# Optimization experiments

Hardware: AMD Instinct MI355X
Metric: run time of the kernel (lower is better)

The kernel has to match this reference:

```python
import jax, jax.numpy as jnp
import numpy as np

B, C, H, W = 2, 256, 32, 32
PK, CK = 256, 256


def setup_inputs() -> dict:
    key = jax.random.key(0)
    ks = jax.random.split(key, 9)
    s = 1.0 / np.sqrt(C)
    return {
        'x': jax.random.normal(ks[0], (B, C, H, W), jnp.float32),
        'primary_indices': jax.random.randint(ks[1], (B, PK), 0, B * H * W),
        'compare_indices': jax.random.randint(ks[2], (B, CK), 0, B * H * W),
        'pre_w': jax.random.uniform(ks[3], (3, C, C), jnp.float32, -s, s),
        'pre_b': jax.random.uniform(ks[4], (3, C), jnp.float32, -s, s),
        'post_w': jax.random.uniform(ks[5], (2, C, C), jnp.float32, -s, s),
        'post_b': jax.random.uniform(ks[6], (2, C), jnp.float32, -s, s),
        'post_out_w': jax.random.uniform(ks[7], (2, C), jnp.float32, -s, s),
        'post_out_b': jax.random.uniform(ks[8], (2,), jnp.float32, -s, s),
    }


def reference(x, primary_indices, compare_indices, pre_w, pre_b,
              post_w, post_b, post_out_w, post_out_b):
    # pre_compare: stack of 1x1 convs (c->c->c->c), ReLU between layers
    h = x
    for i in range(3):
        h = jnp.einsum('bchw,oc->bohw', h, pre_w[i]) + pre_b[i][None, :, None, None]
        if i < 2:
            h = jax.nn.relu(h)
    bs, c, hh, ww = h.shape
    # flatten to [bs*h*w, c] node features (matches torch transpose+reshape)
    flat = h.reshape(bs, c, hh * ww).transpose(0, 2, 1).reshape(bs * hh * ww, c)
    # gather primary / compare node features with global flat indices
    xp = flat[primary_indices.reshape(-1)].reshape(bs, -1, c).transpose(0, 2, 1)  # [b,c,pk]
    xc = flat[compare_indices.reshape(-1)].reshape(bs, -1, c).transpose(0, 2, 1)  # [b,c,ck]
    # broadcast pairwise squared difference -> [b,c,pk,ck]
    xx = (xp[:, :, :, None] - xc[:, :, None, :]) ** 2
    # post_compare: 1x1 conv stack c->c->c->2, ReLU between layers
    g = xx
    for i in range(2):
        g = jax.nn.relu(jnp.einsum('bcpq,oc->bopq', g, post_w[i]) + post_b[i][None, :, None, None])
    out = jnp.einsum('bcpq,oc->bopq', g, post_out_w) + post_out_b[None, :, None, None]
    return out  # [b, 2, pk, ck]
```

## Files before the change

kernel.cpp:

```cpp
#include <hip/hip_runtime.h>

typedef unsigned short u16;
typedef short bf16x8 __attribute__((ext_vector_type(8)));
typedef float f32x4 __attribute__((ext_vector_type(4)));
typedef u16 u16x4 __attribute__((ext_vector_type(4)));

__device__ __forceinline__ float b2f(u16 h) {
  unsigned u = ((unsigned)h) << 16;
  return __builtin_bit_cast(float, u);
}
__device__ __forceinline__ u16 f2b(float f) {
  return __builtin_bit_cast(u16, (__bf16)f);
}
__device__ __forceinline__ void gld_lds16(const void* g, void* l) {
  __builtin_amdgcn_global_load_lds(
      (__attribute__((address_space(1))) void*)(g),
      (__attribute__((address_space(3))) void*)(l), 16, 0, 0);
}

__global__ void dense_edge_prep(const float* __restrict__ x,
                                const float* __restrict__ pre_w,
                                const float* __restrict__ post_w,
                                u16* __restrict__ wb, u16* __restrict__ xt) {
  const int blk = blockIdx.x;
  const int t = threadIdx.x;
  if (blk < 160) {
    const int id = blk * 256 + t;
    const int layer = id >> 13;
    const int sid = id & 8191;
    const int m = sid >> 5;
    const int s8 = sid & 31;
    const float* src = (layer < 2) ? (post_w + layer * 65536)
                                   : (pre_w + (layer - 2) * 65536);
    u16* dst = wb + layer * 65536;
    f32x4 a = *(const f32x4*)(src + m * 256 + s8 * 8);
    f32x4 c = *(const f32x4*)(src + m * 256 + s8 * 8 + 4);
    bf16x8 o;
#pragma unroll
    for (int j = 0; j < 4; j++) o[j] = (short)f2b(a[j]);
#pragma unroll
    for (int j = 0; j < 4; j++) o[4 + j] = (short)f2b(c[j]);
    *(bf16x8*)(dst + (s8 * 256 + m) * 8) = o;
  } else {
    __shared__ float tile[32 * 65];
    const int xb = blk - 160;
    const int b = xb >> 7;
    const int ct = (xb >> 4) & 7;
    const int ht = xb & 15;
    const int c0 = ct * 32, hw0 = ht * 64;
#pragma unroll
    for (int rep = 0; rep < 8; rep++) {
      const int idx = rep * 256 + t;
      const int cl = idx >> 6, hl = idx & 63;
      tile[cl * 65 + hl] = x[(b * 256 + c0 + cl) * 1024 + hw0 + hl];
    }
    __syncthreads();
    const int hl = t >> 2, c8 = t & 3;
    bf16x8 o;
#pragma unroll
    for (int i = 0; i < 8; i++) o[i] = (short)f2b(tile[(c8 * 8 + i) * 65 + hl]);
    *(bf16x8*)(xt + (b * 1024 + hw0 + hl) * 256 + c0 + c8 * 8) = o;
  }
}

__global__ __launch_bounds__(256, 2) void dense_edge_pre(
    const u16* __restrict__ xt, const u16* __restrict__ wpre,
    const float* __restrict__ preb, u16* __restrict__ flat) {
  __shared__ u16 feat[2][4096];
  const int t = threadIdx.x;
  const int wv = t >> 6, ln = t & 63;
  const int nb = blockIdx.x * 16;
  const int q4 = ln >> 4, r15 = ln & 15;

#pragma unroll
  for (int i = 0; i < 2; i++) {
    const int slot = wv * 128 + i * 64 + ln;
    const int s8 = slot >> 4, nl = slot & 15;
    gld_lds16(xt + (nb + nl) * 256 + s8 * 8, &feat[0][slot * 8]);
  }
  __syncthreads();

#pragma unroll
  for (int l = 0; l < 3; l++) {
    const u16* wl = wpre + l * 65536;
    f32x4 acc[4];
    f32x4 zero = {0.f, 0.f, 0.f, 0.f};
#pragma unroll
    for (int mt = 0; mt < 4; mt++) acc[mt] = zero;
#pragma unroll
    for (int s = 0; s < 8; s++) {
      bf16x8 bv = *(const bf16x8*)(&feat[l & 1][((s * 4 + q4) * 16 + r15) * 8]);
#pragma unroll
      for (int mt = 0; mt < 4; mt++) {
        bf16x8 av = *(const bf16x8*)(wl + ((s * 4 + q4) * 256 + wv * 64 + mt * 16 + r15) * 8);
        acc[mt] = __builtin_amdgcn_mfma_f32_16x16x32_bf16(av, bv, acc[mt], 0, 0, 0);
      }
    }
    if (l < 2) {
#pragma unroll
      for (int mt = 0; mt < 4; mt++) {
        const int o = wv * 64 + mt * 16 + q4 * 4;
        f32x4 bb = *(const f32x4*)(preb + l * 256 + o);
        u16x4 pk;
#pragma unroll
        for (int r = 0; r < 4; r++) {
          float v = fmaxf(acc[mt][r] + bb[r], 0.f);
          pk[r] = f2b(v);
        }
        *(u16x4*)(&feat[(l + 1) & 1][((o >> 3) * 16 + r15) * 8 + (o & 7)]) = pk;
      }
      __syncthreads();
    } else {
#pragma unroll
      for (int mt = 0; mt < 4; mt++) {
        const int o = wv * 64 + mt * 16 + q4 * 4;
        f32x4 bb = *(const f32x4*)(preb + 512 + o);
        u16x4 pk;
#pragma unroll
        for (int r = 0; r < 4; r++) pk[r] = f2b(acc[mt][r] + bb[r]);
        *(u16x4*)(flat + (nb + r15) * 256 + o) = pk;
      }
    }
  }
}

#define NT 8
__global__ __launch_bounds__(512, 2) void dense_edge_main(
    const u16* __restrict__ flat, const int* __restrict__ pidx,
    const int* __restrict__ cidx, const u16* __restrict__ w1s,
    const u16* __restrict__ w2s, const float* __restrict__ b1,
    const float* __restrict__ b2, const float* __restrict__ w3,
    const float* __restrict__ b3, float* __restrict__ out) {
  __shared__ u16 xxbuf[2][16384];
  __shared__ u16 t1buf[2][16384];
  __shared__ u16 pstage[2048];
  __shared__ u16 qstage[2][2048];
  __shared__ float pbuf[2][8][2][64];

  const int t = threadIdx.x;
  const int wv = t >> 6;
  const int ln = t & 63;
  const int q4 = ln >> 4, r15 = ln & 15;
  const int blk = blockIdx.x;
  const int tile0 = blk * NT;
  const int b = tile0 >> 10;
  const int pt = (tile0 >> 5) & 31;
  const int qt0 = tile0 & 31;
  const int p0 = pt * 8;

  bf16x8 w1f[2][8], w2f[2][8];
#pragma unroll
  for (int s = 0; s < 8; s++)
#pragma unroll
    for (int mt = 0; mt < 2; mt++) {
      const int off = ((s * 4 + q4) * 256 + wv * 32 + mt * 16 + r15) * 8;
      w1f[mt][s] = *(const bf16x8*)(w1s + off);
      w2f[mt][s] = *(const bf16x8*)(w2s + off);
    }

  {
    const int slot = (wv & 3) * 64 + ln;
    const int row = slot & 7, cc = slot >> 3;
    if (wv < 4) {
      const int pn = pidx[b * 256 + p0 + row];
      gld_lds16(flat + pn * 256 + cc * 8, &pstage[slot * 8]);
    } else {
      const int qn = cidx[b * 256 + qt0 * 8 + row];
      gld_lds16(flat + qn * 256 + cc * 8, &qstage[0][slot * 8]);
    }
  }
  __syncthreads();

  const int prow = ln >> 3, qrow = ln & 7;

  {
    const u16* qs = qstage[0];
#pragma unroll
    for (int i = 0; i < 4; i++) {
      const int cc = wv * 4 + i;
      bf16x8 av = *(const bf16x8*)(&pstage[(cc * 8 + prow) * 8]);
      bf16x8 bv = *(const bf16x8*)(&qs[(cc * 8 + qrow) * 8]);
      bf16x8 ov;
#pragma unroll
      for (int jj = 0; jj < 8; jj++) {
        float d = b2f((u16)av[jj]) - b2f((u16)bv[jj]);
        ov[jj] = (short)f2b(d * d);
      }
      *(bf16x8*)(&xxbuf[0][(cc * 64 + ln) * 8]) = ov;
    }
    if (wv >= 4) {
      const int slot = (wv - 4) * 64 + ln;
      const int qn = cidx[b * 256 + (qt0 + 1) * 8 + (slot & 7)];
      gld_lds16(flat + qn * 256 + (slot >> 3) * 8, &qstage[1][slot * 8]);
    }
  }
  __syncthreads();

#pragma unroll 1
  for (int j = 0; j <= NT; j++) {
    if (j < NT - 1) {
      const u16* qs = qstage[(j + 1) & 1];
#pragma unroll
      for (int i = 0; i < 4; i++) {
        const int cc = wv * 4 + i;
        bf16x8 av = *(const bf16x8*)(&pstage[(cc * 8 + prow) * 8]);
        bf16x8 bv = *(const bf16x8*)(&qs[(cc * 8 + qrow) * 8]);
        bf16x8 ov;
#pragma unroll
        for (int jj = 0; jj < 8; jj++) {
          float d = b2f((u16)av[jj]) - b2f((u16)bv[jj]);
          ov[jj] = (short)f2b(d * d);
        }
        *(bf16x8*)(&xxbuf[(j + 1) & 1][(cc * 64 + ln) * 8]) = ov;
      }
    }
    if (j < NT - 2 && wv >= 4) {
      const int slot = (wv - 4) * 64 + ln;
      const int qn = cidx[b * 256 + (qt0 + j + 2) * 8 + (slot & 7)];
      gld_lds16(flat + qn * 256 + (slot >> 3) * 8,
                &qstage[(j + 2) & 1][slot * 8]);
    }
    if (j < NT) {
      const u16* xb = xxbuf[j & 1];
      f32x4 acc[2][4];
      {
        f32x4 zero = {0.f, 0.f, 0.f, 0.f};
#pragma unroll
        for (int mt = 0; mt < 2; mt++)
#pragma unroll
          for (int nt = 0; nt < 4; nt++) acc[mt][nt] = zero;
      }
#pragma unroll
      for (int s = 0; s < 8; s++) {
        bf16x8 bfr[4];
#pragma unroll
        for (int nt = 0; nt < 4; nt++)
          bfr[nt] = *(const bf16x8*)(xb + ((s * 4 + q4) * 64 + nt * 16 + r15) * 8);
#pragma unroll
        for (int mt = 0; mt < 2; mt++)
#pragma unroll
          for (int nt = 0; nt < 4; nt++)
            acc[mt][nt] = __builtin_amdgcn_mfma_f32_16x16x32_bf16(w1f[mt][s], bfr[nt], acc[mt][nt], 0, 0, 0);
      }
#pragma unroll
      for (int mt = 0; mt < 2; mt++) {
        const int o = wv * 32 + mt * 16 + q4 * 4;
        f32x4 bb = *(const f32x4*)(b1 + o);
#pragma unroll
        for (int nt = 0; nt < 4; nt++) {
          const int nn = nt * 16 + r15;
          u16x4 pk;
#pragma unroll
          for (int r = 0; r < 4; r++) {
            float v = fmaxf(acc[mt][nt][r] + bb[r], 0.f);
            pk[r] = f2b(v);
          }
          *(u16x4*)(&t1buf[j & 1][((o >> 3) * 64 + nn) * 8 + (o & 7)]) = pk;
        }
      }
    }
    if (j > 0) {
      const int jm = j - 1;
      const u16* tb = t1buf[jm & 1];
      f32x4 acc[2][4];
      {
        f32x4 zero = {0.f, 0.f, 0.f, 0.f};
#pragma unroll
        for (int mt = 0; mt < 2; mt++)
#pragma unroll
          for (int nt = 0; nt < 4; nt++) acc[mt][nt] = zero;
      }
#pragma unroll
      for (int s = 0; s < 8; s++) {
        bf16x8 bfr[4];
#pragma unroll
        for (int nt = 0; nt < 4; nt++)
          bfr[nt] = *(const bf16x8*)(tb + ((s * 4 + q4) * 64 + nt * 16 + r15) * 8);
#pragma unroll
        for (int mt = 0; mt < 2; mt++)
#pragma unroll
          for (int nt = 0; nt < 4; nt++)
            acc[mt][nt] = __builtin_amdgcn_mfma_f32_16x16x32_bf16(w2f[mt][s], bfr[nt], acc[mt][nt], 0, 0, 0);
      }
      float part[2][4] = {{0.f, 0.f, 0.f, 0.f}, {0.f, 0.f, 0.f, 0.f}};
#pragma unroll
      for (int mt = 0; mt < 2; mt++) {
        const int o = wv * 32 + mt * 16 + q4 * 4;
        f32x4 bb = *(const f32x4*)(b2 + o);
        f32x4 w3a = *(const f32x4*)(w3 + o);
        f32x4 w3b = *(const f32x4*)(w3 + 256 + o);
#pragma unroll
        for (int nt = 0; nt < 4; nt++) {
#pragma unroll
          for (int r = 0; r < 4; r++) {
            float v = fmaxf(acc[mt][nt][r] + bb[r], 0.f);
            part[0][nt] += v * w3a[r];
            part[1][nt] += v * w3b[r];
          }
        }
      }
#pragma unroll
      for (int o3 = 0; o3 < 2; o3++)
#pragma unroll
        for (int nt = 0; nt < 4; nt++) {
          part[o3][nt] += __shfl_xor(part[o3][nt], 16, 64);
          part[o3][nt] += __shfl_xor(part[o3][nt], 32, 64);
        }
      if (q4 == 0) {
#pragma unroll
        for (int o3 = 0; o3 < 2; o3++)
#pragma unroll
          for (int nt = 0; nt < 4; nt++)
            pbuf[jm & 1][wv][o3][nt * 16 + r15] = part[o3][nt];
      }
    }
    if (j >= 2 && t < 128) {
      const int jo = j - 2;
      const int o3 = t >> 6;
      const int n = t & 63;
      float v = b3[o3];
#pragma unroll
      for (int k = 0; k < 8; k++) v += pbuf[jo & 1][k][o3][n];
      out[((b * 2 + o3) * 256 + p0 + (n >> 3)) * 256 + (qt0 + jo) * 8 + (n & 7)] = v;
    }
    __syncthreads();
  }

  if (t < 128) {
    const int jo = NT - 1;
    const int o3 = t >> 6;
    const int n = t & 63;
    float v = b3[o3];
#pragma unroll
    for (int k = 0; k < 8; k++) v += pbuf[jo & 1][k][o3][n];
    out[((b * 2 + o3) * 256 + p0 + (n >> 3)) * 256 + (qt0 + jo) * 8 + (n & 7)] = v;
  }
}

extern "C" void kernel_launch(void* const* d_in, const int* in_sizes, int n_in,
                              void* d_out, int out_size, void* d_ws, size_t ws_size,
                              hipStream_t stream) {
  (void)in_sizes; (void)n_in; (void)out_size; (void)ws_size;
  const float* x          = (const float*)d_in[0];
  const int*   pidx       = (const int*)d_in[1];
  const int*   cidx       = (const int*)d_in[2];
  const float* pre_w      = (const float*)d_in[3];
  const float* pre_b      = (const float*)d_in[4];
  const float* post_w     = (const float*)d_in[5];
  const float* post_b     = (const float*)d_in[6];
  const float* post_out_w = (const float*)d_in[7];
  const float* post_out_b = (const float*)d_in[8];
  float* out = (float*)d_out;

  u16* ws   = (u16*)d_ws;
  u16* wb   = ws;
  u16* w1s  = wb;
  u16* w2s  = wb + 65536;
  u16* wpre = wb + 131072;
  u16* xt   = ws + 327680;
  u16* flat = ws + 851968;

  dense_edge_prep<<<416, 256, 0, stream>>>(x, pre_w, post_w, wb, xt);
  dense_edge_pre<<<128, 256, 0, stream>>>(xt, wpre, pre_b, flat);
  dense_edge_main<<<256, 512, 0, stream>>>(flat, pidx, cidx, w1s, w2s,
                                           post_b, post_b + 256,
                                           post_out_w, post_out_b, out);
}
```

Baseline: 119.5 us.

## Stagger per-wave stage order, raise MFMA priority, and prefetch gather indices

The loop body is split into squared-difference, first GEMM and second GEMM stages. Odd and even waves now run these stages in opposite order, so MFMA-heavy and VALU/LDS-heavy work from different waves can overlap. MFMA loops are wrapped in s_setprio, the primary-row LDS reads are hoisted into registers once, and compare indices are preloaded into registers one step ahead, so the async gather no longer waits on an index load. This costs extra registers and makes per-wave timing between barriers less uniform.

```diff
diff --git a/kernel.cpp b/kernel.cpp
--- a/kernel.cpp
+++ b/kernel.cpp
@@ -158,27 +158,36 @@
       w2f[mt][s] = *(const bf16x8*)(w2s + off);
     }
 
-  {
-    const int slot = (wv & 3) * 64 + ln;
-    const int row = slot & 7, cc = slot >> 3;
-    if (wv < 4) {
-      const int pn = pidx[b * 256 + p0 + row];
-      gld_lds16(flat + pn * 256 + cc * 8, &pstage[slot * 8]);
-    } else {
-      const int qn = cidx[b * 256 + qt0 * 8 + row];
-      gld_lds16(flat + qn * 256 + cc * 8, &qstage[0][slot * 8]);
-    }
+  const int slot4 = (wv & 3) * 64 + ln;
+  const int srow = slot4 & 7, scc = slot4 >> 3;
+  if (wv < 4) {
+    const int pn = pidx[b * 256 + p0 + srow];
+    gld_lds16(flat + pn * 256 + scc * 8, &pstage[slot4 * 8]);
+  } else {
+    const int qn = cidx[b * 256 + qt0 * 8 + srow];
+    gld_lds16(flat + qn * 256 + scc * 8, &qstage[0][slot4 * 8]);
+  }
+  int qn_pro = 0, qn_cur = 0;
+  if (wv >= 4) {
+    qn_pro = cidx[b * 256 + (qt0 + 1) * 8 + srow];
+    qn_cur = cidx[b * 256 + (qt0 + 2) * 8 + srow];
   }
   __syncthreads();
 
   const int prow = ln >> 3, qrow = ln & 7;
 
-  {
-    const u16* qs = qstage[0];
+  bf16x8 pa[4];
+#pragma unroll
+  for (int i = 0; i < 4; i++)
+    pa[i] = *(const bf16x8*)(&pstage[((wv * 4 + i) * 8 + prow) * 8]);
+
+  auto do_xx = [&](int jx) {
+    const u16* qs = qstage[jx & 1];
+    u16* xb = xxbuf[jx & 1];
 #pragma unroll
     for (int i = 0; i < 4; i++) {
       const int cc = wv * 4 + i;
-      bf16x8 av = *(const bf16x8*)(&pstage[(cc * 8 + prow) * 8]);
+      bf16x8 av = pa[i];
       bf16x8 bv = *(const bf16x8*)(&qs[(cc * 8 + qrow) * 8]);
       bf16x8 ov;
 #pragma unroll
@@ -186,134 +195,115 @@
         float d = b2f((u16)av[jj]) - b2f((u16)bv[jj]);
         ov[jj] = (short)f2b(d * d);
       }
-      *(bf16x8*)(&xxbuf[0][(cc * 64 + ln) * 8]) = ov;
-    }
-    if (wv >= 4) {
-      const int slot = (wv - 4) * 64 + ln;
-      const int qn = cidx[b * 256 + (qt0 + 1) * 8 + (slot & 7)];
-      gld_lds16(flat + qn * 256 + (slot >> 3) * 8, &qstage[1][slot * 8]);
-    }
-  }
+      *(bf16x8*)(&xb[(cc * 64 + ln) * 8]) = ov;
+    }
+  };
+
+  auto do_g1 = [&](int jg) {
+    const u16* xb = xxbuf[jg & 1];
+    f32x4 acc[2][4];
+    {
+      f32x4 zero = {0.f, 0.f, 0.f, 0.f};
+#pragma unroll
+      for (int mt = 0; mt < 2; mt++)
+#pragma unroll
+        for (int nt = 0; nt < 4; nt++) acc[mt][nt] = zero;
+    }
+    __builtin_amdgcn_s_setprio(1);
+#pragma unroll
+    for (int s = 0; s < 8; s++) {
+      bf16x8 bfr[4];
+#pragma unroll
+      for (int nt = 0; nt < 4; nt++)
+        bfr[nt] = *(const bf16x8*)(xb + ((s * 4 + q4) * 64 + nt * 16 + r15) * 8);
+#pragma unroll
+      for (int mt = 0; mt < 2; mt++)
+#pragma unroll
+        for (int nt = 0; nt < 4; nt++)
+          acc[mt][nt] = __builtin_amdgcn_mfma_f32_16x16x32_bf16(w1f[mt][s], bfr[nt], acc[mt][nt], 0, 0, 0);
+    }
+    __builtin_amdgcn_s_setprio(0);
+#pragma unroll
+    for (int mt = 0; mt < 2; mt++) {
+      const int o = wv * 32 + mt * 16 + q4 * 4;
+      f32x4 bb = *(const f32x4*)(b1 + o);
+#pragma unroll
+      for (int nt = 0; nt < 4; nt++) {
+        const int nn = nt * 16 + r15;
+        u16x4 pk;
+#pragma unroll
+        for (int r = 0; r < 4; r++) {
+          float v = fmaxf(acc[mt][nt][r] + bb[r], 0.f);
+          pk[r] = f2b(v);
+        }
+        *(u16x4*)(&t1buf[jg & 1][((o >> 3) * 64 + nn) * 8 + (o & 7)]) = pk;
+      }
+    }
+  };
+
+  auto do_g2 = [&](int jg) {
+    const u16* tb = t1buf[jg & 1];
+    f32x4 acc[2][4];
+    {
+      f32x4 zero = {0.f, 0.f, 0.f, 0.f};
+#pragma unroll
+      for (int mt = 0; mt < 2; mt++)
+#pragma unroll
+        for (int nt = 0; nt < 4; nt++) acc[mt][nt] = zero;
+    }
+    __builtin_amdgcn_s_setprio(1);
+#pragma unroll
+    for (int s = 0; s < 8; s++) {
+      bf16x8 bfr[4];
+#pragma unroll
+      for (int nt = 0; nt < 4; nt++)
+        bfr[nt] = *(const bf16x8*)(tb + ((s * 4 + q4) * 64 + nt * 16 + r15) * 8);
+#pragma unroll
+      for (int mt = 0; mt < 2; mt++)
+#pragma unroll
+        for (int nt = 0; nt < 4; nt++)
+          acc[mt][nt] = __builtin_amdgcn_mfma_f32_16x16x32_bf16(w2f[mt][s], bfr[nt], acc[mt][nt], 0, 0, 0);
+    }
+    __builtin_amdgcn_s_setprio(0);
+    float part[2][4] = {{0.f, 0.f, 0.f, 0.f}, {0.f, 0.f, 0.f, 0.f}};
+#pragma unroll
+    for (int mt = 0; mt < 2; mt++) {
+      const int o = wv * 32 + mt * 16 + q4 * 4;
+      f32x4 bb = *(const f32x4*)(b2 + o);
+      f32x4 w3a = *(const f32x4*)(w3 + o);
+      f32x4 w3b = *(const f32x4*)(w3 + 256 + o);
+#pragma unroll
+      for (int nt = 0; nt < 4; nt++) {
+#pragma unroll
+        for (int r = 0; r < 4; r++) {
+          float v = fmaxf(acc[mt][nt][r] + bb[r], 0.f);
+          part[0][nt] += v * w3a[r];
+          part[1][nt] += v * w3b[r];
+        }
+      }
+    }
+#pragma unroll
+    for (int o3 = 0; o3 < 2; o3++)
+#pragma unroll
+      for (int nt = 0; nt < 4; nt++) {
+        part[o3][nt] += __shfl_xor(part[o3][nt], 16, 64);
+        part[o3][nt] += __shfl_xor(part[o3][nt], 32, 64);
+      }
+    if (q4 == 0) {
+#pragma unroll
+      for (int o3 = 0; o3 < 2; o3++)
+#pragma unroll
+        for (int nt = 0; nt < 4; nt++)
+          pbuf[jg & 1][wv][o3][nt * 16 + r15] = part[o3][nt];
+    }
+  };
+
+  do_xx(0);
+  if (wv >= 4) gld_lds16(flat + qn_pro * 256 + scc * 8, &qstage[1][slot4 * 8]);
   __syncthreads();
 
 #pragma unroll 1
   for (int j = 0; j <= NT; j++) {
-    if (j < NT - 1) {
-      const u16* qs = qstage[(j + 1) & 1];
-#pragma unroll
-      for (int i = 0; i < 4; i++) {
-        const int cc = wv * 4 + i;
-        bf16x8 av = *(const bf16x8*)(&pstage[(cc * 8 + prow) * 8]);
-        bf16x8 bv = *(const bf16x8*)(&qs[(cc * 8 + qrow) * 8]);
-        bf16x8 ov;
-#pragma unroll
-        for (int jj = 0; jj < 8; jj++) {
-          float d = b2f((u16)av[jj]) - b2f((u16)bv[jj]);
-          ov[jj] = (short)f2b(d * d);
-        }
-        *(bf16x8*)(&xxbuf[(j + 1) & 1][(cc * 64 + ln) * 8]) = ov;
-      }
-    }
-    if (j < NT - 2 && wv >= 4) {
-      const int slot = (wv - 4) * 64 + ln;
-      const int qn = cidx[b * 256 + (qt0 + j + 2) * 8 + (slot & 7)];
-      gld_lds16(flat + qn * 256 + (slot >> 3) * 8,
-                &qstage[(j + 2) & 1][slot * 8]);
-    }
-    if (j < NT) {
-      const u16* xb = xxbuf[j & 1];
-      f32x4 acc[2][4];
-      {
-        f32x4 zero = {0.f, 0.f, 0.f, 0.f};
-#pragma unroll
-        for (int mt = 0; mt < 2; mt++)
-#pragma unroll
-          for (int nt = 0; nt < 4; nt++) acc[mt][nt] = zero;
-      }
-#pragma unroll
-      for (int s = 0; s < 8; s++) {
-        bf16x8 bfr[4];
-#pragma unroll
-        for (int nt = 0; nt < 4; nt++)
-          bfr[nt] = *(const bf16x8*)(xb + ((s * 4 + q4) * 64 + nt * 16 + r15) * 8);
-#pragma unroll
-        for (int mt = 0; mt < 2; mt++)
-#pragma unroll
-          for (int nt = 0; nt < 4; nt++)
-            acc[mt][nt] = __builtin_amdgcn_mfma_f32_16x16x32_bf16(w1f[mt][s], bfr[nt], acc[mt][nt], 0, 0, 0);
-      }
-#pragma unroll
-      for (int mt = 0; mt < 2; mt++) {
-        const int o = wv * 32 + mt * 16 + q4 * 4;
-        f32x4 bb = *(const f32x4*)(b1 + o);
-#pragma unroll
-        for (int nt = 0; nt < 4; nt++) {
-          const int nn = nt * 16 + r15;
-          u16x4 pk;
-#pragma unroll
-          for (int r = 0; r < 4; r++) {
-            float v = fmaxf(acc[mt][nt][r] + bb[r], 0.f);
-            pk[r] = f2b(v);
-          }
-          *(u16x4*)(&t1buf[j & 1][((o >> 3) * 64 + nn) * 8 + (o & 7)]) = pk;
-        }
-      }
-    }
-    if (j > 0) {
-      const int jm = j - 1;
-      const u16* tb = t1buf[jm & 1];
-      f32x4 acc[2][4];
-      {
-        f32x4 zero = {0.f, 0.f, 0.f, 0.f};
-#pragma unroll
-        for (int mt = 0; mt < 2; mt++)
-#pragma unroll
-          for (int nt = 0; nt < 4; nt++) acc[mt][nt] = zero;
-      }
-#pragma unroll
-      for (int s = 0; s < 8; s++) {
-        bf16x8 bfr[4];
-#pragma unroll
-        for (int nt = 0; nt < 4; nt++)
-          bfr[nt] = *(const bf16x8*)(tb + ((s * 4 + q4) * 64 + nt * 16 + r15) * 8);
-#pragma unroll
-        for (int mt = 0; mt < 2; mt++)
-#pragma unroll
-          for (int nt = 0; nt < 4; nt++)
-            acc[mt][nt] = __builtin_amdgcn_mfma_f32_16x16x32_bf16(w2f[mt][s], bfr[nt], acc[mt][nt], 0, 0, 0);
-      }
-      float part[2][4] = {{0.f, 0.f, 0.f, 0.f}, {0.f, 0.f, 0.f, 0.f}};
-#pragma unroll
-      for (int mt = 0; mt < 2; mt++) {
-        const int o = wv * 32 + mt * 16 + q4 * 4;
-        f32x4 bb = *(const f32x4*)(b2 + o);
-        f32x4 w3a = *(const f32x4*)(w3 + o);
-        f32x4 w3b = *(const f32x4*)(w3 + 256 + o);
-#pragma unroll
-        for (int nt = 0; nt < 4; nt++) {
-#pragma unroll
-          for (int r = 0; r < 4; r++) {
-            float v = fmaxf(acc[mt][nt][r] + bb[r], 0.f);
-            part[0][nt] += v * w3a[r];
-            part[1][nt] += v * w3b[r];
-          }
-        }
-      }
-#pragma unroll
-      for (int o3 = 0; o3 < 2; o3++)
-#pragma unroll
-        for (int nt = 0; nt < 4; nt++) {
-          part[o3][nt] += __shfl_xor(part[o3][nt], 16, 64);
-          part[o3][nt] += __shfl_xor(part[o3][nt], 32, 64);
-        }
-      if (q4 == 0) {
-#pragma unroll
-        for (int o3 = 0; o3 < 2; o3++)
-#pragma unroll
-          for (int nt = 0; nt < 4; nt++)
-            pbuf[jm & 1][wv][o3][nt * 16 + r15] = part[o3][nt];
-      }
-    }
     if (j >= 2 && t < 128) {
       const int jo = j - 2;
       const int o3 = t >> 6;
@@ -322,6 +312,19 @@
 #pragma unroll
       for (int k = 0; k < 8; k++) v += pbuf[jo & 1][k][o3][n];
       out[((b * 2 + o3) * 256 + p0 + (n >> 3)) * 256 + (qt0 + jo) * 8 + (n & 7)] = v;
+    }
+    if (j < NT - 2 && wv >= 4) {
+      gld_lds16(flat + qn_cur * 256 + scc * 8, &qstage[j & 1][slot4 * 8]);
+      if (j < NT - 3) qn_cur = cidx[b * 256 + (qt0 + j + 3) * 8 + srow];
+    }
+    if (wv & 1) {
+      if (j < NT - 1) do_xx(j + 1);
+      if (j > 0) do_g2(j - 1);
+      if (j < NT) do_g1(j);
+    } else {
+      if (j < NT) do_g1(j);
+      if (j > 0) do_g2(j - 1);
+      if (j < NT - 1) do_xx(j + 1);
     }
     __syncthreads();
   }
```

Result: no change. 117.2 us (-1.9%).
